# Performance work log

Measured on AMD Instinct MI355X. Metric: run time of the kernel, lower is better.

## Reference

```python
import jax, jax.numpy as jnp
import numpy as np

D = 2048
H = 16
DK = D // H
B = 2
S = 2048


def setup_inputs() -> dict:
    key = jax.random.key(0)
    ks = jax.random.split(key, 11)
    s = 1.0 / np.sqrt(D)
    inp = {
        "q": jax.random.normal(ks[0], (B, S, D), jnp.float32),
        "k": jax.random.normal(ks[1], (B, S, D), jnp.float32),
        "v": jax.random.normal(ks[2], (B, S, D), jnp.float32),
        "mask": 0,
        "Wq": jax.random.normal(ks[3], (D, D), jnp.float32) * s,
        "bq": jax.random.normal(ks[4], (D,), jnp.float32) * s,
        "Wk": jax.random.normal(ks[5], (D, D), jnp.float32) * s,
        "bk": jax.random.normal(ks[6], (D,), jnp.float32) * s,
        "Wv": jax.random.normal(ks[7], (D, D), jnp.float32) * s,
        "bv": jax.random.normal(ks[8], (D,), jnp.float32) * s,
        "Wo": jax.random.normal(ks[9], (D, D), jnp.float32) * s,
        "bo": jax.random.normal(ks[10], (D,), jnp.float32) * s,
    }
    return inp


def reference(q, k, v, mask, Wq, bq, Wk, bk, Wv, bv, Wo, bo):
    # Linear projections (torch Linear: x @ W.T + b)
    query = q @ Wq.T + bq  # [B,S,D]
    key_ = k @ Wk.T + bk
    value = v @ Wv.T + bv
    # split heads -> [B,S,H,DK]
    query = query.reshape(B, S, H, DK)
    key_ = key_.reshape(B, S, H, DK)
    value = value.reshape(B, S, H, DK)
    # scores [B,H,Sq,Sk]
    scores = jnp.einsum('nqhd,nkhd->nhqk', query, key_)
    if mask:
        # faithful to source: fill where triu(ones, diag=1) == 0 (lower tri incl diag)
        tri = jnp.triu(jnp.ones((S, S), jnp.float32), k=1)
        scores = jnp.where(tri == 0, jnp.float32(-1e20), scores)
    attn = jax.nn.softmax(scores / np.sqrt(DK), axis=3)
    # dropout=0.0 -> identity
    out = jnp.einsum('nhql,nlhd->nqhd', attn, value).reshape(B, S, D)
    return out @ Wo.T + bo
```

## Files before the change

kernel.cpp:

```cpp
#include <hip/hip_runtime.h>
#include <math.h>

typedef unsigned short u16;
typedef u16 u16x8 __attribute__((ext_vector_type(8)));
typedef u16 u16x4 __attribute__((ext_vector_type(4)));
typedef short s16x8 __attribute__((ext_vector_type(8)));
typedef short s16x4 __attribute__((ext_vector_type(4)));
typedef float f32x4 __attribute__((ext_vector_type(4)));
typedef float f32x16 __attribute__((ext_vector_type(16)));

static constexpr int B_ = 2;
static constexpr int S_ = 2048;
static constexpr int D_ = 2048;
static constexpr int H_ = 16;
static constexpr int DK = 128;
static constexpr long long BSD = (long long)B_ * S_ * D_;
static constexpr long long DD  = (long long)D_ * D_;

#if __has_builtin(__builtin_amdgcn_mfma_f32_32x32x16_bf16)
#define HAVE_MFMA3232 1
#else
#define HAVE_MFMA3232 0
#endif
#if __has_builtin(__builtin_amdgcn_mfma_f32_16x16x32_bf16)
#define HAVE_MFMA32 1
#else
#define HAVE_MFMA32 0
#endif
#if __has_builtin(__builtin_amdgcn_mfma_f32_16x16x16bf16_1k)
#define HAVE_MFMA16 1
#else
#define HAVE_MFMA16 0
#endif

__device__ __forceinline__ u16 f2bf(float f) {
    union { float f; unsigned u; } cv; cv.f = f;
    unsigned u = cv.u;
    return (u16)((u + 0x7fffu + ((u >> 16) & 1u)) >> 16);
}

__device__ __forceinline__ unsigned pack2bf(float a, float b) {
    union { float f; unsigned u; } x, y; x.f = a; y.f = b;
    return ((y.u + 0x8000u) & 0xffff0000u) | ((x.u + 0x8000u) >> 16);
}

__device__ __forceinline__ f32x16 mfma3232(f32x16 c, u16x8 a, u16x8 b) {
#if HAVE_MFMA3232
    return __builtin_amdgcn_mfma_f32_32x32x16_bf16((s16x8)a, (s16x8)b, c, 0, 0, 0);
#else
    asm volatile("v_mfma_f32_32x32x16_bf16 %0, %1, %2, %0" : "+v"(c) : "v"(a), "v"(b));
    return c;
#endif
}
__device__ __forceinline__ f32x4 mfma32(f32x4 c, u16x8 a, u16x8 b) {
#if HAVE_MFMA32
    return __builtin_amdgcn_mfma_f32_16x16x32_bf16((s16x8)a, (s16x8)b, c, 0, 0, 0);
#else
    asm volatile("v_mfma_f32_16x16x32_bf16 %0, %1, %2, %0" : "+v"(c) : "v"(a), "v"(b));
    return c;
#endif
}
__device__ __forceinline__ f32x4 mfma16(f32x4 c, u16x4 a, u16x4 b) {
#if HAVE_MFMA16
    return __builtin_amdgcn_mfma_f32_16x16x16bf16_1k((s16x4)a, (s16x4)b, c, 0, 0, 0);
#else
    asm volatile("v_mfma_f32_16x16x16_bf16 %0, %1, %2, %0" : "+v"(c) : "v"(a), "v"(b));
    return c;
#endif
}
__device__ __forceinline__ void fenceA() {
#if !HAVE_MFMA3232
    asm volatile("s_nop 7\ns_nop 7" :::);
#endif
}
__device__ __forceinline__ void fenceB() {
#if !HAVE_MFMA32 || !HAVE_MFMA16
    asm volatile("s_nop 7\ns_nop 7" :::);
#endif
}

__device__ __forceinline__ void glds16(const u16* g, u16* l) {
    __builtin_amdgcn_global_load_lds(
        (const __attribute__((address_space(1))) unsigned int*)g,
        (__attribute__((address_space(3))) unsigned int*)l, 16, 0, 0);
}

__device__ __forceinline__ float fexp2(float x) {
#if __has_builtin(__builtin_amdgcn_exp2f)
    return __builtin_amdgcn_exp2f(x);
#else
    return exp2f(x);
#endif
}

struct CastArgs {
    const float* src[7];
    u16* dst[7];
    int start[8];
};
__global__ __launch_bounds__(256) void cast_all(CastArgs a) {
    int g = blockIdx.x * 256 + threadIdx.x;
    if (g >= a.start[7]) return;
    int seg = 0;
#pragma unroll
    for (int i = 1; i < 7; ++i) seg += (g >= a.start[i]) ? 1 : 0;
    int idx = g - a.start[seg];
    float4 f = ((const float4*)a.src[seg])[idx];
    ushort4 o;
    o.x = f2bf(f.x); o.y = f2bf(f.y); o.z = f2bf(f.z); o.w = f2bf(f.w);
    ((ushort4*)a.dst[seg])[idx] = o;
}

struct QkvArgs {
    const u16* X[3];
    const u16* W[3];
    const float* bias[3];
    u16* outQ;
    u16* outK;
    u16* outVt;
    float scaleQ;
};
__global__ __launch_bounds__(256) void qkv_proj(QkvArgs a) {
    __shared__ u16 SM[8704];
    u16* As = SM;
    u16* Bs = SM + 4096;

    const int zsel = blockIdx.z;
    const u16* A = a.X[zsel];
    const u16* Bw = a.W[zsel];
    const float scale = (zsel == 0) ? a.scaleQ : 1.0f;

    const int t = threadIdx.x;
    const int wave = t >> 6, lane = t & 63;
    const int l32 = lane & 31, lhi = lane >> 5;
    const int wm = (wave >> 1) * 64;
    const int wn = (wave & 1) * 64;
    const long long m0 = (long long)blockIdx.y * 128;
    const long long n0 = (long long)blockIdx.x * 128;

    f32x16 acc[2][2];
#pragma unroll
    for (int i = 0; i < 2; ++i)
#pragma unroll
        for (int j = 0; j < 2; ++j)
            acc[i][j] = (f32x16)(0.f);

    for (int k0 = 0; k0 < D_; k0 += 32) {
        __syncthreads();
#pragma unroll
        for (int s = 0; s < 2; ++s) {
            int slot = s * 256 + t;
            int row = slot >> 2;
            int c = (t & 3) ^ ((row >> 1) & 3);
            glds16(A + (m0 + row) * D_ + k0 + c * 8, &As[slot * 8]);
        }
#pragma unroll
        for (int s = 0; s < 2; ++s) {
            int slot = s * 256 + t;
            int row = slot >> 2;
            int c = (t & 3) ^ ((row >> 1) & 3);
            glds16(Bw + (n0 + row) * D_ + k0 + c * 8, &Bs[slot * 8]);
        }
        __syncthreads();

        u16x8 af[2][2], bf[2][2];
#pragma unroll
        for (int i = 0; i < 2; ++i)
#pragma unroll
            for (int kk = 0; kk < 2; ++kk) {
                int row = wm + i * 32 + l32;
                int c = (kk * 2 + lhi) ^ ((row >> 1) & 3);
                af[i][kk] = *(const u16x8*)(&As[row * 32 + c * 8]);
            }
#pragma unroll
        for (int j = 0; j < 2; ++j)
#pragma unroll
            for (int kk = 0; kk < 2; ++kk) {
                int row = wn + j * 32 + l32;
                int c = (kk * 2 + lhi) ^ ((row >> 1) & 3);
                bf[j][kk] = *(const u16x8*)(&Bs[row * 32 + c * 8]);
            }
#pragma unroll
        for (int kk = 0; kk < 2; ++kk)
#pragma unroll
            for (int i = 0; i < 2; ++i)
#pragma unroll
                for (int j = 0; j < 2; ++j)
                    acc[i][j] = mfma3232(acc[i][j], af[i][kk], bf[j][kk]);
    }

    fenceA();

    float bs[2];
#pragma unroll
    for (int j = 0; j < 2; ++j)
        bs[j] = a.bias[zsel][(int)n0 + wn + j * 32 + l32];

    if (zsel < 2) {
        u16* C = (zsel == 0) ? a.outQ : a.outK;
#pragma unroll
        for (int p = 0; p < 2; ++p) {
            __syncthreads();
            int lc = (wave & 1) * 32 + l32;
#pragma unroll
            for (int i = 0; i < 2; ++i)
#pragma unroll
                for (int r = 0; r < 16; ++r) {
                    int row = wm + i * 32 + 4 * lhi + (r & 3) + 8 * (r >> 2);
                    SM[row * 64 + lc] = f2bf((acc[i][p][r] + bs[p]) * scale);
                }
            __syncthreads();
#pragma unroll
            for (int i = 0; i < 4; ++i) {
                int idx = i * 256 + t;
                int row = idx >> 3, cc = idx & 7;
                u16x8 val = *(const u16x8*)(&SM[row * 64 + cc * 8]);
                long long n = n0 + 32 * p + (cc & 3) * 8 + (cc >> 2) * 64;
                *(u16x8*)(C + (m0 + row) * (long long)D_ + n) = val;
            }
        }
    } else {
        const int h = blockIdx.x;
        const int b = (int)(m0 >> 11);
        const int tok0 = (int)(m0 & 2047);
        const int z = b * 16 + h;
        u16* vt = a.outVt + (long long)z * DK * S_;
#pragma unroll
        for (int p = 0; p < 2; ++p) {
            __syncthreads();
            int lc = (wave & 1) * 32 + l32;
#pragma unroll
            for (int i = 0; i < 2; ++i)
#pragma unroll
                for (int r = 0; r < 16; ++r) {
                    int row = wm + i * 32 + 4 * lhi + (r & 3) + 8 * (r >> 2);
                    SM[lc * 136 + row] = f2bf(acc[i][p][r] + bs[p]);
                }
            __syncthreads();
#pragma unroll
            for (int i = 0; i < 4; ++i) {
                int idx = i * 256 + t;
                int lc2 = idx >> 4, cc = idx & 15;
                int d = p * 32 + (lc2 & 31) + (lc2 >> 5) * 64;
                u16x8 val = *(const u16x8*)(&SM[lc2 * 136 + cc * 8]);
                *(u16x8*)(vt + (long long)d * S_ + tok0 + cc * 8) = val;
            }
        }
    }
}

__global__ __launch_bounds__(256) void gemm_out(const u16* __restrict__ A,
                                                const u16* __restrict__ B,
                                                float* __restrict__ C,
                                                const float* __restrict__ bias) {
    __shared__ u16 SM[16384];
    u16* As = SM;
    u16* Bs = SM + 4096;

    const int t = threadIdx.x;
    const int wave = t >> 6, lane = t & 63;
    const int l32 = lane & 31, lhi = lane >> 5;
    const int wm = (wave >> 1) * 64;
    const int wn = (wave & 1) * 64;
    const long long m0 = (long long)blockIdx.y * 128;
    const long long n0 = (long long)blockIdx.x * 128;

    f32x16 acc[2][2];
#pragma unroll
    for (int i = 0; i < 2; ++i)
#pragma unroll
        for (int j = 0; j < 2; ++j)
            acc[i][j] = (f32x16)(0.f);

    for (int k0 = 0; k0 < D_; k0 += 32) {
        __syncthreads();
#pragma unroll
        for (int s = 0; s < 2; ++s) {
            int slot = s * 256 + t;
            int row = slot >> 2;
            int c = (t & 3) ^ ((row >> 1) & 3);
            glds16(A + (m0 + row) * D_ + k0 + c * 8, &As[slot * 8]);
        }
#pragma unroll
        for (int s = 0; s < 2; ++s) {
            int slot = s * 256 + t;
            int row = slot >> 2;
            int c = (t & 3) ^ ((row >> 1) & 3);
            glds16(B + (n0 + row) * D_ + k0 + c * 8, &Bs[slot * 8]);
        }
        __syncthreads();

        u16x8 af[2][2], bf[2][2];
#pragma unroll
        for (int i = 0; i < 2; ++i)
#pragma unroll
            for (int kk = 0; kk < 2; ++kk) {
                int row = wm + i * 32 + l32;
                int c = (kk * 2 + lhi) ^ ((row >> 1) & 3);
                af[i][kk] = *(const u16x8*)(&As[row * 32 + c * 8]);
            }
#pragma unroll
        for (int j = 0; j < 2; ++j)
#pragma unroll
            for (int kk = 0; kk < 2; ++kk) {
                int row = wn + j * 32 + l32;
                int c = (kk * 2 + lhi) ^ ((row >> 1) & 3);
                bf[j][kk] = *(const u16x8*)(&Bs[row * 32 + c * 8]);
            }
#pragma unroll
        for (int kk = 0; kk < 2; ++kk)
#pragma unroll
            for (int i = 0; i < 2; ++i)
#pragma unroll
                for (int j = 0; j < 2; ++j)
                    acc[i][j] = mfma3232(acc[i][j], af[i][kk], bf[j][kk]);
    }

    fenceA();

    float bs[2];
#pragma unroll
    for (int j = 0; j < 2; ++j)
        bs[j] = bias[(int)n0 + wn + j * 32 + l32];

    float* Cf = (float*)SM;
#pragma unroll
    for (int p = 0; p < 2; ++p) {
        __syncthreads();
        int lc = (wave & 1) * 32 + l32;
#pragma unroll
        for (int i = 0; i < 2; ++i)
#pragma unroll
            for (int r = 0; r < 16; ++r) {
                int row = wm + i * 32 + 4 * lhi + (r & 3) + 8 * (r >> 2);
                Cf[row * 64 + lc] = acc[i][p][r] + bs[p];
            }
        __syncthreads();
#pragma unroll
        for (int i = 0; i < 8; ++i) {
            int idx = i * 256 + t;
            int row = idx >> 4, c4 = idx & 15;
            f32x4 val = *(const f32x4*)(&Cf[row * 64 + c4 * 4]);
            long long n = n0 + (c4 >> 3) * 64 + p * 32 + (c4 & 7) * 4;
            *(f32x4*)(C + (m0 + row) * (long long)D_ + n) = val;
        }
    }
}

__global__ __launch_bounds__(256, 2) void flash_attn(const u16* __restrict__ Qb,
                                                     const u16* __restrict__ Kb,
                                                     const u16* __restrict__ Vt,
                                                     u16* __restrict__ Ob) {
    __shared__ u16 Ks[2][64 * 128];
    __shared__ u16 Vs[2][128 * 64];

    const int z  = blockIdx.x;
    const int qt = blockIdx.y;
    const int b  = z >> 4, h = z & 15;
    const int t = threadIdx.x, wave = t >> 6, lane = t & 63;
    const int quad = lane >> 4, l16 = lane & 15;

    const u16* kbase = Kb + (long long)(b * S_) * D_ + h * DK;
    const u16* vbase = Vt + (long long)z * DK * S_;

    u16x8 qf[2][4];
    {
        const u16* qbase = Qb + ((long long)(b * S_ + qt * 128 + wave * 32 + l16)) * D_
                              + h * DK + quad * 8;
#pragma unroll
        for (int jq = 0; jq < 2; ++jq)
#pragma unroll
            for (int kk = 0; kk < 4; ++kk)
                qf[jq][kk] = *(const u16x8*)(qbase + (long long)jq * 16 * D_ + kk * 32);
    }

    f32x4 acc_o[2][8];
#pragma unroll
    for (int jq = 0; jq < 2; ++jq)
#pragma unroll
        for (int jd = 0; jd < 8; ++jd)
            acc_o[jq][jd] = f32x4{0.f, 0.f, 0.f, 0.f};
    float l_[2] = {0.f, 0.f};

    u16x8 vreg[4];

    {
#pragma unroll
        for (int i = 0; i < 4; ++i) {
            int slot = i * 256 + t;
            int row = slot >> 3, c16 = slot & 7;
            vreg[i] = *(const u16x8*)(vbase + (long long)row * S_ + c16 * 8);
        }
#pragma unroll
        for (int i = 0; i < 4; ++i) {
            int slot = i * 256 + t;
            int row = slot >> 4;
            int cs = (slot & 15) ^ (row & 7);
            glds16(kbase + (long long)row * D_ + cs * 8, &Ks[0][slot * 8]);
        }
#pragma unroll
        for (int i = 0; i < 4; ++i) {
            int slot = i * 256 + t;
            int row = slot >> 3, c16 = slot & 7;
            int rm = row & 15;
            u16x4 lo = __builtin_shufflevector(vreg[i], vreg[i], 0, 1, 2, 3);
            u16x4 hi = __builtin_shufflevector(vreg[i], vreg[i], 4, 5, 6, 7);
            *(u16x4*)(&Vs[0][row * 64 + (((2 * c16) ^ rm) * 4)]) = lo;
            *(u16x4*)(&Vs[0][row * 64 + (((2 * c16 + 1) ^ rm) * 4)]) = hi;
        }
    }

    for (int kt = 0; kt < S_ / 64; ++kt) {
        __syncthreads();
        const int p = kt & 1;
        const u16* ks = Ks[p];
        const u16* vs = Vs[p];
        const bool pre = (kt + 1) < (S_ / 64);
        if (pre) {
            const u16* vsrc = vbase + (kt + 1) * 64;
#pragma unroll
            for (int i = 0; i < 4; ++i) {
                int slot = i * 256 + t;
                int row = slot >> 3, c16 = slot & 7;
                vreg[i] = *(const u16x8*)(vsrc + (long long)row * S_ + c16 * 8);
            }
            const u16* ksrc = kbase + (long long)(kt + 1) * 64 * D_;
#pragma unroll
            for (int i = 0; i < 4; ++i) {
                int slot = i * 256 + t;
                int row = slot >> 4;
                int cs = (slot & 15) ^ (row & 7);
                glds16(ksrc + (long long)row * D_ + cs * 8, &Ks[p ^ 1][slot * 8]);
            }
        }

        f32x4 st[4][2];
#pragma unroll
        for (int ik = 0; ik < 4; ++ik)
#pragma unroll
            for (int jq = 0; jq < 2; ++jq)
                st[ik][jq] = f32x4{0.f, 0.f, 0.f, 0.f};
#pragma unroll
        for (int kk = 0; kk < 4; ++kk) {
            u16x8 kf[4];
#pragma unroll
            for (int ik = 0; ik < 4; ++ik) {
                int krow = ik * 16 + l16;
                kf[ik] = *(const u16x8*)(&ks[krow * 128 + (((kk * 4 + quad) ^ (l16 & 7)) * 8)]);
            }
#pragma unroll
            for (int ik = 0; ik < 4; ++ik) {
                st[ik][0] = mfma32(st[ik][0], kf[ik], qf[0][kk]);
                st[ik][1] = mfma32(st[ik][1], kf[ik], qf[1][kk]);
            }
        }
        fenceB();

        if (pre) {
#pragma unroll
            for (int i = 0; i < 4; ++i) {
                int slot = i * 256 + t;
                int row = slot >> 3, c16 = slot & 7;
                int rm = row & 15;
                u16x4 lo = __builtin_shufflevector(vreg[i], vreg[i], 0, 1, 2, 3);
                u16x4 hi = __builtin_shufflevector(vreg[i], vreg[i], 4, 5, 6, 7);
                *(u16x4*)(&Vs[p ^ 1][row * 64 + (((2 * c16) ^ rm) * 4)]) = lo;
                *(u16x4*)(&Vs[p ^ 1][row * 64 + (((2 * c16 + 1) ^ rm) * 4)]) = hi;
            }
        }

        u16x4 pf[4][2];
#pragma unroll
        for (int ik = 0; ik < 4; ++ik)
#pragma unroll
            for (int jq = 0; jq < 2; ++jq) {
                float p0 = fexp2(st[ik][jq][0]);
                float p1 = fexp2(st[ik][jq][1]);
                float p2 = fexp2(st[ik][jq][2]);
                float p3 = fexp2(st[ik][jq][3]);
                l_[jq] += (p0 + p1) + (p2 + p3);
                union { u16x4 v; unsigned u[2]; } pk;
                pk.u[0] = pack2bf(p0, p1);
                pk.u[1] = pack2bf(p2, p3);
                pf[ik][jq] = pk.v;
            }

#pragma unroll
        for (int ik = 0; ik < 4; ++ik) {
            const int kc = ik * 4 + quad;
            u16x4 vf[8];
#pragma unroll
            for (int jd = 0; jd < 8; ++jd) {
                int vrow = jd * 16 + l16;
                vf[jd] = *(const u16x4*)(&vs[vrow * 64 + ((kc ^ l16) * 4)]);
            }
#pragma unroll
            for (int jd = 0; jd < 8; ++jd) {
                acc_o[0][jd] = mfma16(acc_o[0][jd], pf[ik][0], vf[jd]);
                acc_o[1][jd] = mfma16(acc_o[1][jd], pf[ik][1], vf[jd]);
            }
        }
        fenceB();
    }

    float lr[2][4];
#pragma unroll
    for (int jq = 0; jq < 2; ++jq) {
        float s = l_[jq];
        s += __shfl_xor(s, 16, 64);
        s += __shfl_xor(s, 32, 64);
        float inv = 1.f / s;
#pragma unroll
        for (int r = 0; r < 4; ++r)
            lr[jq][r] = __shfl(inv, quad * 20 + r, 64);
    }
    u16* OS = (u16*)Ks;
    __syncthreads();
#pragma unroll
    for (int jq = 0; jq < 2; ++jq)
#pragma unroll
        for (int r = 0; r < 4; ++r) {
            int qloc = wave * 32 + jq * 16 + quad * 4 + r;
#pragma unroll
            for (int jd = 0; jd < 8; ++jd)
                OS[qloc * 128 + jd * 16 + l16] = f2bf(acc_o[jq][jd][r] * lr[jq][r]);
        }
    __syncthreads();
    u16* obase = Ob + ((long long)(b * S_ + qt * 128)) * D_ + h * DK;
#pragma unroll
    for (int i = 0; i < 8; ++i) {
        int idx = i * 256 + t;
        int row = idx >> 4, cc = idx & 15;
        *(u16x8*)(obase + (long long)row * D_ + cc * 8) = *(const u16x8*)(&OS[row * 128 + cc * 8]);
    }
}

extern "C" void kernel_launch(void* const* d_in, const int* in_sizes, int n_in,
                              void* d_out, int out_size, void* d_ws, size_t ws_size,
                              hipStream_t stream) {
    const float* q  = (const float*)d_in[0];
    const float* k  = (const float*)d_in[1];
    const float* v  = (const float*)d_in[2];
    const float* Wq = (const float*)d_in[4];
    const float* bq = (const float*)d_in[5];
    const float* Wk = (const float*)d_in[6];
    const float* bk = (const float*)d_in[7];
    const float* Wv = (const float*)d_in[8];
    const float* bv = (const float*)d_in[9];
    const float* Wo = (const float*)d_in[10];
    const float* bo = (const float*)d_in[11];
    float* out = (float*)d_out;

    u16* ws = (u16*)d_ws;
    u16* xq  = ws; ws += BSD;
    u16* xk  = ws; ws += BSD;
    u16* xv  = ws; ws += BSD;
    u16* wqb = ws; ws += DD;
    u16* wkb = ws; ws += DD;
    u16* wvb = ws; ws += DD;
    u16* wob = ws; ws += DD;
    u16* Qb  = ws; ws += BSD;
    u16* Kb  = ws; ws += BSD;
    u16* Vt  = ws; ws += BSD;
    u16* Ob  = ws; ws += BSD;

    const float q_scale = (float)(0.08838834764831845 * 1.4426950408889634);

    {
        CastArgs a;
        const float* srcs[7] = {q, k, v, Wq, Wk, Wv, Wo};
        u16* dsts[7] = {xq, xk, xv, wqb, wkb, wvb, wob};
        int n4s[7] = {(int)(BSD / 4), (int)(BSD / 4), (int)(BSD / 4),
                      (int)(DD / 4), (int)(DD / 4), (int)(DD / 4), (int)(DD / 4)};
        int acc = 0;
        for (int i = 0; i < 7; ++i) { a.src[i] = srcs[i]; a.dst[i] = dsts[i]; a.start[i] = acc; acc += n4s[i]; }
        a.start[7] = acc;
        cast_all<<<(acc + 255) / 256, 256, 0, stream>>>(a);
    }

    {
        QkvArgs a;
        a.X[0] = xq;  a.X[1] = xk;  a.X[2] = xv;
        a.W[0] = wqb; a.W[1] = wkb; a.W[2] = wvb;
        a.bias[0] = bq; a.bias[1] = bk; a.bias[2] = bv;
        a.outQ = Qb; a.outK = Kb; a.outVt = Vt;
        a.scaleQ = q_scale;
        qkv_proj<<<dim3(D_ / 128, (B_ * S_) / 128, 3), 256, 0, stream>>>(a);
    }

    flash_attn<<<dim3(B_ * H_, S_ / 128), 256, 0, stream>>>(Qb, Kb, Vt, Ob);

    gemm_out<<<dim3(D_ / 128, (B_ * S_) / 128), 256, 0, stream>>>(Ob, wob, out, bo);
}
```

Baseline: 464.7 us.

## Switch projection GEMMs to 16x16x32 MFMA with BK=64 tiles

Both the QKV projection and output GEMMs now use 16x16x32 bf16 MFMA tiles (4x4 per wave) instead of 32x32x16, with the K step doubled to 64 and a matching XOR swizzle on the LDS layout. Each iteration loads twice as much data per barrier pair, halving the loop count and synchronisation overhead. The cost is more LDS (32 KB per block for QKV), which may reduce occupancy, plus more fragment loads per MFMA and different epilogue indexing.

```diff
diff --git a/kernel.cpp b/kernel.cpp
--- a/kernel.cpp
+++ b/kernel.cpp
@@ -7,7 +7,6 @@
 typedef short s16x8 __attribute__((ext_vector_type(8)));
 typedef short s16x4 __attribute__((ext_vector_type(4)));
 typedef float f32x4 __attribute__((ext_vector_type(4)));
-typedef float f32x16 __attribute__((ext_vector_type(16)));
 
 static constexpr int B_ = 2;
 static constexpr int S_ = 2048;
@@ -17,11 +16,6 @@
 static constexpr long long BSD = (long long)B_ * S_ * D_;
 static constexpr long long DD  = (long long)D_ * D_;
 
-#if __has_builtin(__builtin_amdgcn_mfma_f32_32x32x16_bf16)
-#define HAVE_MFMA3232 1
-#else
-#define HAVE_MFMA3232 0
-#endif
 #if __has_builtin(__builtin_amdgcn_mfma_f32_16x16x32_bf16)
 #define HAVE_MFMA32 1
 #else
@@ -44,14 +38,6 @@
     return ((y.u + 0x8000u) & 0xffff0000u) | ((x.u + 0x8000u) >> 16);
 }
 
-__device__ __forceinline__ f32x16 mfma3232(f32x16 c, u16x8 a, u16x8 b) {
-#if HAVE_MFMA3232
-    return __builtin_amdgcn_mfma_f32_32x32x16_bf16((s16x8)a, (s16x8)b, c, 0, 0, 0);
-#else
-    asm volatile("v_mfma_f32_32x32x16_bf16 %0, %1, %2, %0" : "+v"(c) : "v"(a), "v"(b));
-    return c;
-#endif
-}
 __device__ __forceinline__ f32x4 mfma32(f32x4 c, u16x8 a, u16x8 b) {
 #if HAVE_MFMA32
     return __builtin_amdgcn_mfma_f32_16x16x32_bf16((s16x8)a, (s16x8)b, c, 0, 0, 0);
@@ -66,11 +52,6 @@
 #else
     asm volatile("v_mfma_f32_16x16x16_bf16 %0, %1, %2, %0" : "+v"(c) : "v"(a), "v"(b));
     return c;
-#endif
-}
-__device__ __forceinline__ void fenceA() {
-#if !HAVE_MFMA3232
-    asm volatile("s_nop 7\ns_nop 7" :::);
 #endif
 }
 __device__ __forceinline__ void fenceB() {
@@ -110,6 +91,50 @@
     o.x = f2bf(f.x); o.y = f2bf(f.y); o.z = f2bf(f.z); o.w = f2bf(f.w);
     ((ushort4*)a.dst[seg])[idx] = o;
 }
+
+#define GEMM_K64_LOOP(Aptr, Bptr)                                                   \
+    for (int k0 = 0; k0 < D_; k0 += 64) {                                           \
+        __syncthreads();                                                            \
+        _Pragma("unroll")                                                           \
+        for (int s = 0; s < 4; ++s) {                                               \
+            int slot = s * 256 + t;                                                 \
+            int row = slot >> 3;                                                    \
+            int c = (t & 7) ^ (row & 7);                                            \
+            glds16(Aptr + (m0 + row) * D_ + k0 + c * 8, &As[slot * 8]);             \
+        }                                                                           \
+        _Pragma("unroll")                                                           \
+        for (int s = 0; s < 4; ++s) {                                               \
+            int slot = s * 256 + t;                                                 \
+            int row = slot >> 3;                                                    \
+            int c = (t & 7) ^ (row & 7);                                            \
+            glds16(Bptr + (n0 + row) * D_ + k0 + c * 8, &Bs[slot * 8]);             \
+        }                                                                           \
+        __syncthreads();                                                            \
+        u16x8 af[4][2], bf[4][2];                                                   \
+        _Pragma("unroll")                                                           \
+        for (int i = 0; i < 4; ++i) {                                               \
+            int row = wm + i * 16 + l16;                                            \
+            _Pragma("unroll")                                                       \
+            for (int kk = 0; kk < 2; ++kk)                                          \
+                af[i][kk] = *(const u16x8*)(&As[row * 64 +                          \
+                                (((kk * 4 + quad) ^ (row & 7)) * 8)]);              \
+        }                                                                           \
+        _Pragma("unroll")                                                           \
+        for (int j = 0; j < 4; ++j) {                                               \
+            int row = wn + j * 16 + l16;                                            \
+            _Pragma("unroll")                                                       \
+            for (int kk = 0; kk < 2; ++kk)                                          \
+                bf[j][kk] = *(const u16x8*)(&Bs[row * 64 +                          \
+                                (((kk * 4 + quad) ^ (row & 7)) * 8)]);              \
+        }                                                                           \
+        _Pragma("unroll")                                                           \
+        for (int kk = 0; kk < 2; ++kk)                                              \
+            _Pragma("unroll")                                                       \
+            for (int i = 0; i < 4; ++i)                                             \
+                _Pragma("unroll")                                                   \
+                for (int j = 0; j < 4; ++j)                                         \
+                    acc[i][j] = mfma32(acc[i][j], af[i][kk], bf[j][kk]);            \
+    }
 
 struct QkvArgs {
     const u16* X[3];
@@ -121,9 +146,9 @@
     float scaleQ;
 };
 __global__ __launch_bounds__(256) void qkv_proj(QkvArgs a) {
-    __shared__ u16 SM[8704];
+    __shared__ u16 SM[16384];
     u16* As = SM;
-    u16* Bs = SM + 4096;
+    u16* Bs = SM + 8192;
 
     const int zsel = blockIdx.z;
     const u16* A = a.X[zsel];
@@ -132,83 +157,45 @@
 
     const int t = threadIdx.x;
     const int wave = t >> 6, lane = t & 63;
-    const int l32 = lane & 31, lhi = lane >> 5;
+    const int quad = lane >> 4, l16 = lane & 15;
     const int wm = (wave >> 1) * 64;
     const int wn = (wave & 1) * 64;
     const long long m0 = (long long)blockIdx.y * 128;
     const long long n0 = (long long)blockIdx.x * 128;
 
-    f32x16 acc[2][2];
-#pragma unroll
-    for (int i = 0; i < 2; ++i)
-#pragma unroll
-        for (int j = 0; j < 2; ++j)
-            acc[i][j] = (f32x16)(0.f);
-
-    for (int k0 = 0; k0 < D_; k0 += 32) {
-        __syncthreads();
-#pragma unroll
-        for (int s = 0; s < 2; ++s) {
-            int slot = s * 256 + t;
-            int row = slot >> 2;
-            int c = (t & 3) ^ ((row >> 1) & 3);
-            glds16(A + (m0 + row) * D_ + k0 + c * 8, &As[slot * 8]);
-        }
-#pragma unroll
-        for (int s = 0; s < 2; ++s) {
-            int slot = s * 256 + t;
-            int row = slot >> 2;
-            int c = (t & 3) ^ ((row >> 1) & 3);
-            glds16(Bw + (n0 + row) * D_ + k0 + c * 8, &Bs[slot * 8]);
-        }
-        __syncthreads();
-
-        u16x8 af[2][2], bf[2][2];
-#pragma unroll
-        for (int i = 0; i < 2; ++i)
-#pragma unroll
-            for (int kk = 0; kk < 2; ++kk) {
-                int row = wm + i * 32 + l32;
-                int c = (kk * 2 + lhi) ^ ((row >> 1) & 3);
-                af[i][kk] = *(const u16x8*)(&As[row * 32 + c * 8]);
-            }
-#pragma unroll
-        for (int j = 0; j < 2; ++j)
-#pragma unroll
-            for (int kk = 0; kk < 2; ++kk) {
-                int row = wn + j * 32 + l32;
-                int c = (kk * 2 + lhi) ^ ((row >> 1) & 3);
-                bf[j][kk] = *(const u16x8*)(&Bs[row * 32 + c * 8]);
-            }
-#pragma unroll
-        for (int kk = 0; kk < 2; ++kk)
-#pragma unroll
-            for (int i = 0; i < 2; ++i)
-#pragma unroll
-                for (int j = 0; j < 2; ++j)
-                    acc[i][j] = mfma3232(acc[i][j], af[i][kk], bf[j][kk]);
-    }
-
-    fenceA();
-
-    float bs[2];
-#pragma unroll
-    for (int j = 0; j < 2; ++j)
-        bs[j] = a.bias[zsel][(int)n0 + wn + j * 32 + l32];
+    f32x4 acc[4][4];
+#pragma unroll
+    for (int i = 0; i < 4; ++i)
+#pragma unroll
+        for (int j = 0; j < 4; ++j)
+            acc[i][j] = f32x4{0.f, 0.f, 0.f, 0.f};
+
+    GEMM_K64_LOOP(A, Bw)
+
+    fenceB();
+
+    float bs[4];
+#pragma unroll
+    for (int j = 0; j < 4; ++j)
+        bs[j] = a.bias[zsel][(int)n0 + wn + j * 16 + l16];
 
     if (zsel < 2) {
         u16* C = (zsel == 0) ? a.outQ : a.outK;
 #pragma unroll
         for (int p = 0; p < 2; ++p) {
             __syncthreads();
-            int lc = (wave & 1) * 32 + l32;
-#pragma unroll
-            for (int i = 0; i < 2; ++i)
-#pragma unroll
-                for (int r = 0; r < 16; ++r) {
-                    int row = wm + i * 32 + 4 * lhi + (r & 3) + 8 * (r >> 2);
-                    SM[row * 64 + lc] = f2bf((acc[i][p][r] + bs[p]) * scale);
-                }
+#pragma unroll
+            for (int jj = 0; jj < 2; ++jj) {
+                int j = p * 2 + jj;
+#pragma unroll
+                for (int i = 0; i < 4; ++i)
+#pragma unroll
+                    for (int r = 0; r < 4; ++r) {
+                        int row = wm + i * 16 + quad * 4 + r;
+                        int lc = (wave & 1) * 32 + jj * 16 + l16;
+                        SM[row * 64 + lc] = f2bf((acc[i][j][r] + bs[j]) * scale);
+                    }
+            }
             __syncthreads();
 #pragma unroll
             for (int i = 0; i < 4; ++i) {
@@ -228,14 +215,18 @@
 #pragma unroll
         for (int p = 0; p < 2; ++p) {
             __syncthreads();
-            int lc = (wave & 1) * 32 + l32;
-#pragma unroll
-            for (int i = 0; i < 2; ++i)
-#pragma unroll
-                for (int r = 0; r < 16; ++r) {
-                    int row = wm + i * 32 + 4 * lhi + (r & 3) + 8 * (r >> 2);
-                    SM[lc * 136 + row] = f2bf(acc[i][p][r] + bs[p]);
-                }
+#pragma unroll
+            for (int jj = 0; jj < 2; ++jj) {
+                int j = p * 2 + jj;
+#pragma unroll
+                for (int i = 0; i < 4; ++i)
+#pragma unroll
+                    for (int r = 0; r < 4; ++r) {
+                        int row = wm + i * 16 + quad * 4 + r;
+                        int lc = (wave & 1) * 32 + jj * 16 + l16;
+                        SM[lc * 136 + row] = f2bf(acc[i][j][r] + bs[j]);
+                    }
+            }
             __syncthreads();
 #pragma unroll
             for (int i = 0; i < 4; ++i) {
@@ -249,92 +240,54 @@
     }
 }
 
-__global__ __launch_bounds__(256) void gemm_out(const u16* __restrict__ A,
-                                                const u16* __restrict__ B,
+__global__ __launch_bounds__(256) void gemm_out(const u16* __restrict__ Ain,
+                                                const u16* __restrict__ Bin,
                                                 float* __restrict__ C,
                                                 const float* __restrict__ bias) {
     __shared__ u16 SM[16384];
     u16* As = SM;
-    u16* Bs = SM + 4096;
+    u16* Bs = SM + 8192;
 
     const int t = threadIdx.x;
     const int wave = t >> 6, lane = t & 63;
-    const int l32 = lane & 31, lhi = lane >> 5;
+    const int quad = lane >> 4, l16 = lane & 15;
     const int wm = (wave >> 1) * 64;
     const int wn = (wave & 1) * 64;
     const long long m0 = (long long)blockIdx.y * 128;
     const long long n0 = (long long)blockIdx.x * 128;
 
-    f32x16 acc[2][2];
-#pragma unroll
-    for (int i = 0; i < 2; ++i)
-#pragma unroll
-        for (int j = 0; j < 2; ++j)
-            acc[i][j] = (f32x16)(0.f);
-
-    for (int k0 = 0; k0 < D_; k0 += 32) {
-        __syncthreads();
-#pragma unroll
-        for (int s = 0; s < 2; ++s) {
-            int slot = s * 256 + t;
-            int row = slot >> 2;
-            int c = (t & 3) ^ ((row >> 1) & 3);
-            glds16(A + (m0 + row) * D_ + k0 + c * 8, &As[slot * 8]);
-        }
-#pragma unroll
-        for (int s = 0; s < 2; ++s) {
-            int slot = s * 256 + t;
-            int row = slot >> 2;
-            int c = (t & 3) ^ ((row >> 1) & 3);
-            glds16(B + (n0 + row) * D_ + k0 + c * 8, &Bs[slot * 8]);
-        }
-        __syncthreads();
-
-        u16x8 af[2][2], bf[2][2];
-#pragma unroll
-        for (int i = 0; i < 2; ++i)
-#pragma unroll
-            for (int kk = 0; kk < 2; ++kk) {
-                int row = wm + i * 32 + l32;
-                int c = (kk * 2 + lhi) ^ ((row >> 1) & 3);
-                af[i][kk] = *(const u16x8*)(&As[row * 32 + c * 8]);
-            }
-#pragma unroll
-        for (int j = 0; j < 2; ++j)
-#pragma unroll
-            for (int kk = 0; kk < 2; ++kk) {
-                int row = wn + j * 32 + l32;
-                int c = (kk * 2 + lhi) ^ ((row >> 1) & 3);
-                bf[j][kk] = *(const u16x8*)(&Bs[row * 32 + c * 8]);
-            }
-#pragma unroll
-        for (int kk = 0; kk < 2; ++kk)
-#pragma unroll
-            for (int i = 0; i < 2; ++i)
-#pragma unroll
-                for (int j = 0; j < 2; ++j)
-                    acc[i][j] = mfma3232(acc[i][j], af[i][kk], bf[j][kk]);
-    }
-
-    fenceA();
-
-    float bs[2];
-#pragma unroll
-    for (int j = 0; j < 2; ++j)
-        bs[j] = bias[(int)n0 + wn + j * 32 + l32];
+    f32x4 acc[4][4];
+#pragma unroll
+    for (int i = 0; i < 4; ++i)
+#pragma unroll
+        for (int j = 0; j < 4; ++j)
+            acc[i][j] = f32x4{0.f, 0.f, 0.f, 0.f};
+
+    GEMM_K64_LOOP(Ain, Bin)
+
+    fenceB();
+
+    float bs[4];
+#pragma unroll
+    for (int j = 0; j < 4; ++j)
+        bs[j] = bias[(int)n0 + wn + j * 16 + l16];
 
     float* Cf = (float*)SM;
 #pragma unroll
     for (int p = 0; p < 2; ++p) {
         __syncthreads();
-        int lc = (wave & 1) * 32 + l32;
-#pragma unroll
-        for (int i = 0; i < 2; ++i)
-#pragma unroll
-            for (int r = 0; r < 16; ++r) {
-                int row = wm + i * 32 + 4 * lhi + (r & 3) + 8 * (r >> 2);
-                Cf[row * 64 + lc] = acc[i][p][r] + bs[p];
-            }
+#pragma unroll
+        for (int jj = 0; jj < 2; ++jj) {
+            int j = p * 2 + jj;
+#pragma unroll
+            for (int i = 0; i < 4; ++i)
+#pragma unroll
+                for (int r = 0; r < 4; ++r) {
+                    int row = wm + i * 16 + quad * 4 + r;
+                    int lc = (wave & 1) * 32 + jj * 16 + l16;
+                    Cf[row * 64 + lc] = acc[i][j][r] + bs[j];
+                }
+        }
         __syncthreads();
 #pragma unroll
         for (int i = 0; i < 8; ++i) {
```

Measured after the change: 446.7 us. 1.04x faster.
